# Kernel tuning notes

Hardware: AMD Instinct MI355X
Metric: run time of the kernel (lower is better)

The kernel has to match this reference:

```python
import jax, jax.numpy as jnp
import numpy as np

D_MODEL = 512
NHEAD = 8
D_K = D_MODEL // NHEAD


def setup_inputs() -> dict:
    key = jax.random.key(0)
    ks = jax.random.split(key, 11)
    B, N = 2, 16384
    s = 1.0 / np.sqrt(D_MODEL)
    inp = {
        "query": jax.random.normal(ks[0], (B, N, D_MODEL), jnp.float32),
        "key": jax.random.normal(ks[1], (B, N, D_MODEL), jnp.float32),
        "value": jax.random.normal(ks[2], (B, N, D_MODEL), jnp.float32),
        "Wq": jax.random.normal(ks[3], (D_MODEL, D_MODEL), jnp.float32) * s,
        "bq": jnp.zeros((D_MODEL,), jnp.float32),
        "Wk": jax.random.normal(ks[4], (D_MODEL, D_MODEL), jnp.float32) * s,
        "bk": jnp.zeros((D_MODEL,), jnp.float32),
        "Wv": jax.random.normal(ks[5], (D_MODEL, D_MODEL), jnp.float32) * s,
        "bv": jnp.zeros((D_MODEL,), jnp.float32),
        "Wo": jax.random.normal(ks[6], (D_MODEL, D_MODEL), jnp.float32) * s,
        "bo": jnp.zeros((D_MODEL,), jnp.float32),
    }
    return inp


def _split_heads(x):
    # [b, n, d_model] -> [b, h, n, d_k]
    b, n, _ = x.shape
    return x.reshape(b, n, NHEAD, D_K).transpose(0, 2, 1, 3)


def reference(query, key, value, Wq, bq, Wk, bk, Wv, bv, Wo, bo):
    b, n, _ = query.shape
    q = _split_heads(query @ Wq + bq)  # [b,h,n,dk]
    k = _split_heads(key @ Wk + bk)
    v = _split_heads(value @ Wv + bv)

    # linear attention (Shen et al. 2018): softmax over feature dim of q,
    # softmax over sequence dim of k, then KV outer-product context.
    q = jax.nn.softmax(q, axis=-1) / jnp.sqrt(jnp.asarray(D_K, q.dtype))
    k = jax.nn.softmax(k, axis=-2)
    context = jnp.einsum('bhnd,bhne->bhde', k, v)   # [b,h,dk,dk]
    out = jnp.einsum('bhnd,bhde->bhne', q, context)  # [b,h,n,dk]

    out = out.transpose(0, 2, 1, 3).reshape(b, n, D_MODEL)
    return out @ Wo + bo
```

## Files before the change

kernel.cpp:

```cpp
#include <hip/hip_runtime.h>
#include <hip/hip_bf16.h>


using u16 = unsigned short;
typedef __attribute__((ext_vector_type(8))) short bf16x8;
typedef __attribute__((ext_vector_type(4))) float f32x4;

#define D_MODEL 512
#define SEQ 16384


#define PART_OFF 0u
#define SUMS_OFF 16777216u
#define CTX_OFF  17039360u
#define WTKS_OFF 17301504u
#define WTVS_OFF 17825792u
#define WTQS_OFF 18350080u
#define MTS_OFF  18874368u
#define WS_NEEDED 19922944u

__device__ __forceinline__ float bf2f(u16 u) {
  union { unsigned int i; float f; } x; x.i = ((unsigned int)u) << 16; return x.f;
}
__device__ __forceinline__ u16 f2bf(float f) {
  union { float ff; unsigned int i; } x; x.ff = f;
  unsigned int r = x.i + 0x7fffu + ((x.i >> 16) & 1u);
  return (u16)(r >> 16);
}
__device__ __forceinline__ unsigned int pk2(float lo, float hi) {
  union { __hip_bfloat162 h; unsigned int u; } x;
  x.h = __float22bfloat162_rn(float2{lo, hi});
  return x.u;
}
__device__ __forceinline__ bf16x8 ldsrd(const u16* base, int row, int rowbytes,
                                        int kbyte, int mask) {
  return *(const bf16x8*)((const char*)base + row * rowbytes + (kbyte ^ ((row & mask) << 4)));
}
__device__ __forceinline__ void bar_lgkm() {
  asm volatile("s_waitcnt lgkmcnt(0)" ::: "memory");
  __builtin_amdgcn_sched_barrier(0);
  __builtin_amdgcn_s_barrier();
  __builtin_amdgcn_sched_barrier(0);
}

__launch_bounds__(256)
__global__ void wcvt_kernel(const float* __restrict__ Wk, const float* __restrict__ Wv,
                            const float* __restrict__ Wq, u16* __restrict__ WTks,
                            u16* __restrict__ WTvs, u16* __restrict__ WTqs) {
  const float* in = blockIdx.z == 0 ? Wk : (blockIdx.z == 1 ? Wv : Wq);
  u16* out = blockIdx.z == 0 ? WTks : (blockIdx.z == 1 ? WTvs : WTqs);
  __shared__ float S[64][65];
  const int t = threadIdx.x;
  const int k0 = blockIdx.y << 6, c0 = blockIdx.x << 6;
#pragma unroll
  for (int ii = 0; ii < 4; ++ii) {
    const int idx = t + ii * 256;
    const int r = idx >> 4, c4 = (idx & 15) << 2;
    const float4 v = *(const float4*)(in + (k0 + r) * D_MODEL + c0 + c4);
    S[r][c4] = v.x; S[r][c4 + 1] = v.y; S[r][c4 + 2] = v.z; S[r][c4 + 3] = v.w;
  }
  __syncthreads();
#pragma unroll
  for (int it = 0; it < 2; ++it) {
    const int fi = it * 256 + t;
    const int cb_loc = fi >> 7;
    const int ksm_loc = (fi >> 6) & 1;
    const int lane = fi & 63;
    const int col_loc = cb_loc * 16 + (lane & 15);
    const int kl0 = ksm_loc * 32 + (lane >> 4) * 8;
    union { bf16x8 v; u16 e[8]; } o;
#pragma unroll
    for (int jj = 0; jj < 8; ++jj) o.e[jj] = f2bf(S[kl0 + jj][col_loc]);
    const int cb16 = blockIdx.x * 4 + cb_loc;
    const int ksm = blockIdx.y * 2 + ksm_loc;
    *(bf16x8*)(out + cb16 * 8192 + ksm * 512 + lane * 8) = o.v;
  }
}

__launch_bounds__(512, 4)
__global__ void phase1_kernel(const float* __restrict__ key, const float* __restrict__ value,
                              const u16* __restrict__ WTks, const u16* __restrict__ WTvs,
                              const float* __restrict__ bkp, const float* __restrict__ bvp,
                              float* __restrict__ part, float* __restrict__ sums) {
  __shared__ __align__(16) u16 smem[40960];
  u16* KA = smem;
  u16* VA = smem + 16384;
  u16* ET = smem + 32768;
  u16* VT = smem + 36864;
  const int t = threadIdx.x;
  const int lane = t & 63, w = t >> 6;
  const int g = lane >> 4, lc = lane & 15;
  const int f = blockIdx.x;
  const int jj = f >> 3, xc = f & 7;
  const int hp = jj & 3;
  const int y = xc * 16 + (jj >> 2);
  const int hloc = w >> 2, cq = w & 3;
  const int h = hp * 2 + hloc;
  const int dl = cq * 16 + lc;
  const int b = y >> 6, grp = y & 63;
  const int bh = b * 8 + h;
  u16* ETh = ET + hloc * 2048;
  u16* VTh = VT + hloc * 2048;
  const u16* wtkb = WTks + (h * 4 + cq) * 8192;
  const u16* wtvb = WTvs + (h * 4 + cq) * 8192;
  const float bbk = bkp[h * 64 + dl];
  const float bbv = bvp[h * 64 + dl];
  const int srow = t >> 4, sc8 = t & 15;
  const int swoff = srow * 1024 + ((sc8 << 3) ^ ((srow & 7) << 4));

  f32x4 pacc[4];
#pragma unroll
  for (int em = 0; em < 4; ++em) pacc[em] = (f32x4){0.f, 0.f, 0.f, 0.f};
  float sp = 0.f;
  bf16x8 bB[16];

#pragma unroll 1
  for (int ci = 0; ci < 8; ++ci) {
    const int n0 = (y * 8 + ci) * 32;
    {
      const float* kp = key + (size_t)(n0 + srow) * D_MODEL + sc8 * 4;
      const float* vp = value + (size_t)(n0 + srow) * D_MODEL + sc8 * 4;
      float4 lk[8], lv[8];
#pragma unroll
      for (int q = 0; q < 8; ++q) lk[q] = *(const float4*)(kp + q * 64);
#pragma unroll
      for (int q = 0; q < 8; ++q) lv[q] = *(const float4*)(vp + q * 64);
#pragma unroll
      for (int q = 0; q < 8; ++q) {
        *(uint2*)((char*)KA + swoff + q * 128) =
            make_uint2(pk2(lk[q].x, lk[q].y), pk2(lk[q].z, lk[q].w));
        *(uint2*)((char*)VA + swoff + q * 128) =
            make_uint2(pk2(lv[q].x, lv[q].y), pk2(lv[q].z, lv[q].w));
      }
    }
    bar_lgkm();

#pragma unroll
    for (int ks = 0; ks < 16; ++ks) bB[ks] = *(const bf16x8*)(wtkb + ks * 512 + lane * 8);
    f32x4 a0 = (f32x4){0.f, 0.f, 0.f, 0.f}, a1 = a0;
#pragma unroll
    for (int ks = 0; ks < 16; ++ks) {
      const int kb = ks * 64 + g * 16;
      bf16x8 ak0 = ldsrd(KA, lc, 1024, kb, 7);
      bf16x8 ak1 = ldsrd(KA, 16 + lc, 1024, kb, 7);
      a0 = __builtin_amdgcn_mfma_f32_16x16x32_bf16(ak0, bB[ks], a0, 0, 0, 0);
      a1 = __builtin_amdgcn_mfma_f32_16x16x32_bf16(ak1, bB[ks], a1, 0, 0, 0);
    }
    {
#pragma unroll
      for (int r = 0; r < 4; ++r) { a0[r] = __expf(a0[r] + bbk); sp += a0[r]; }
#pragma unroll
      for (int r = 0; r < 4; ++r) { a1[r] = __expf(a1[r] + bbk); sp += a1[r]; }
      *(uint2*)((char*)ETh + dl * 64 + ((g * 8) ^ ((dl & 3) << 4))) =
          make_uint2(pk2(a0[0], a0[1]), pk2(a0[2], a0[3]));
      *(uint2*)((char*)ETh + dl * 64 + ((32 + g * 8) ^ ((dl & 3) << 4))) =
          make_uint2(pk2(a1[0], a1[1]), pk2(a1[2], a1[3]));
    }
#pragma unroll
    for (int ks = 0; ks < 16; ++ks) bB[ks] = *(const bf16x8*)(wtvb + ks * 512 + lane * 8);
    a0 = (f32x4){0.f, 0.f, 0.f, 0.f}; a1 = a0;
#pragma unroll
    for (int ks = 0; ks < 16; ++ks) {
      const int kb = ks * 64 + g * 16;
      bf16x8 av0 = ldsrd(VA, lc, 1024, kb, 7);
      bf16x8 av1 = ldsrd(VA, 16 + lc, 1024, kb, 7);
      a0 = __builtin_amdgcn_mfma_f32_16x16x32_bf16(av0, bB[ks], a0, 0, 0, 0);
      a1 = __builtin_amdgcn_mfma_f32_16x16x32_bf16(av1, bB[ks], a1, 0, 0, 0);
    }
    *(uint2*)((char*)VTh + dl * 64 + ((g * 8) ^ ((dl & 3) << 4))) =
        make_uint2(pk2(a0[0] + bbv, a0[1] + bbv), pk2(a0[2] + bbv, a0[3] + bbv));
    *(uint2*)((char*)VTh + dl * 64 + ((32 + g * 8) ^ ((dl & 3) << 4))) =
        make_uint2(pk2(a1[0] + bbv, a1[1] + bbv), pk2(a1[2] + bbv, a1[3] + bbv));
    bar_lgkm();

    {
      bf16x8 paf = ldsrd(ETh, dl, 64, g * 16, 3);
#pragma unroll
      for (int em = 0; em < 4; ++em) {
        bf16x8 pbf = ldsrd(VTh, em * 16 + lc, 64, g * 16, 3);
        pacc[em] = __builtin_amdgcn_mfma_f32_16x16x32_bf16(paf, pbf, pacc[em], 0, 0, 0);
      }
    }
    bar_lgkm();
  }

  float* pp = part + (size_t)(bh * 64 + grp) * 4096;
#pragma unroll
  for (int em = 0; em < 4; ++em)
    *(f32x4*)(pp + (em * 16 + lc) * 64 + cq * 16 + g * 4) = pacc[em];
  sp += __shfl_xor(sp, 16); sp += __shfl_xor(sp, 32);
  if (g == 0) sums[(size_t)(bh * 64 + grp) * 64 + dl] = sp;
}

__launch_bounds__(256)
__global__ void reduce_kernel(const float* __restrict__ part, const float* __restrict__ sums,
                              float* __restrict__ ctx) {
  __shared__ float den[64];
  const int bh = blockIdx.x;
  const int t = threadIdx.x;
  if (t < 64) {
    float s = 0.f;
    for (int gp = 0; gp < 64; ++gp) s += sums[(size_t)(bh * 64 + gp) * 64 + t];
    den[t] = s;
  }
  float4 A0 = {0,0,0,0}, A1 = {0,0,0,0}, A2 = {0,0,0,0}, A3 = {0,0,0,0};
  const float* pb = part + (size_t)bh * 64 * 4096;
  for (int gp = 0; gp < 64; ++gp) {
    const float4* q = (const float4*)(pb + gp * 4096 + t * 16);
    const float4 q0 = q[0], q1 = q[1], q2 = q[2], q3 = q[3];
    A0.x += q0.x; A0.y += q0.y; A0.z += q0.z; A0.w += q0.w;
    A1.x += q1.x; A1.y += q1.y; A1.z += q1.z; A1.w += q1.w;
    A2.x += q2.x; A2.y += q2.y; A2.z += q2.z; A2.w += q2.w;
    A3.x += q3.x; A3.y += q3.y; A3.z += q3.z; A3.w += q3.w;
  }
  __syncthreads();
  const int e = t >> 2, d0 = (t & 3) * 16;
  float* cb = ctx + (size_t)bh * 4096 + e;
  const float r0[4] = {A0.x, A0.y, A0.z, A0.w};
  const float r1[4] = {A1.x, A1.y, A1.z, A1.w};
  const float r2[4] = {A2.x, A2.y, A2.z, A2.w};
  const float r3[4] = {A3.x, A3.y, A3.z, A3.w};
#pragma unroll
  for (int i = 0; i < 4; ++i) cb[(d0 + i) * 64] = r0[i] / den[d0 + i];
#pragma unroll
  for (int i = 0; i < 4; ++i) cb[(d0 + 4 + i) * 64] = r1[i] / den[d0 + 4 + i];
#pragma unroll
  for (int i = 0; i < 4; ++i) cb[(d0 + 8 + i) * 64] = r2[i] / den[d0 + 8 + i];
#pragma unroll
  for (int i = 0; i < 4; ++i) cb[(d0 + 12 + i) * 64] = r3[i] / den[d0 + 12 + i];
}

__launch_bounds__(256)
__global__ void mbigT_kernel(const float* __restrict__ ctx, const float* __restrict__ Wo,
                             u16* __restrict__ MTs) {
  __shared__ float Clds[64][65];
  __shared__ float Wlds2[64][64];
  const int t = threadIdx.x;
  const int tx = t & 15, ty = t >> 4;
  const int cc = blockIdx.x;
  const int bh = blockIdx.y;
  const int b = bh >> 3, h = bh & 7;
  const float* ch = ctx + bh * 4096;
  for (int i4 = t; i4 < 1024; i4 += 256) {
    const int r = i4 >> 4, c = (i4 & 15) << 2;
    const float4 v = *(const float4*)(ch + (r << 6) + c);
    Clds[r][c] = v.x; Clds[r][c + 1] = v.y; Clds[r][c + 2] = v.z; Clds[r][c + 3] = v.w;
    const float4 wv = *(const float4*)(Wo + (h * 64 + r) * D_MODEL + cc * 64 + c);
    Wlds2[r][c] = wv.x; Wlds2[r][c + 1] = wv.y; Wlds2[r][c + 2] = wv.z; Wlds2[r][c + 3] = wv.w;
  }
  __syncthreads();
  float acc[4][4] = {};
#pragma unroll 8
  for (int k = 0; k < 64; ++k) {
    float a[4], wv[4];
#pragma unroll
    for (int i = 0; i < 4; ++i) a[i] = Clds[(ty << 2) + i][k];
#pragma unroll
    for (int j = 0; j < 4; ++j) wv[j] = Wlds2[k][(tx << 2) + j];
#pragma unroll
    for (int i = 0; i < 4; ++i)
#pragma unroll
      for (int j = 0; j < 4; ++j) acc[i][j] = fmaf(a[i], wv[j], acc[i][j]);
  }
#pragma unroll
  for (int i = 0; i < 4; ++i)
#pragma unroll
    for (int j = 0; j < 4; ++j) {
      const int c = cc * 64 + (tx << 2) + j;
      const int k = h * 64 + (ty << 2) + i;
      const int cb16 = c >> 4, lcc = c & 15;
      const int ksm = k >> 5, gg = (k >> 3) & 3, jb = k & 7;
      MTs[(size_t)b * 262144 + cb16 * 8192 + ksm * 512 + (gg * 16 + lcc) * 8 + jb]
          = f2bf(acc[i][j]);
    }
}

__launch_bounds__(512, 2)
__global__ void phase3_kernel(const float* __restrict__ query, const u16* __restrict__ WTqs,
                              const float* __restrict__ bqp, const u16* __restrict__ MTs,
                              const float* __restrict__ bop, float* __restrict__ out) {
  __shared__ __align__(16) u16 smem[20480];
  u16* SL = smem;
  u16* P  = smem + 4096;
  const int t = threadIdx.x;
  const int lane = t & 63, w = t >> 6;
  const int g = lane >> 4, lc = lane & 15;
  const int chunk = blockIdx.x;
  const int n0 = chunk * 32;
  const int b = chunk >> 9;
  const int c0 = w * 64;
  const int srow = t >> 4;
  const int scol = (t & 15) << 2;
  const int sbyte = srow * 128 + (((t & 15) << 3) ^ ((srow & 7) << 4));
  const float* qbase = query + (size_t)(n0 + srow) * D_MODEL + scol;

  float4 lq[2];
  f32x4 acc[4][2];
#pragma unroll
  for (int m = 0; m < 4; ++m)
#pragma unroll
    for (int n = 0; n < 2; ++n) acc[m][n] = (f32x4){0.f, 0.f, 0.f, 0.f};

  lq[0] = *(const float4*)(qbase);
  lq[1] = *(const float4*)(qbase + 64);
  *(uint2*)((char*)SL + sbyte) = make_uint2(pk2(lq[0].x, lq[0].y), pk2(lq[0].z, lq[0].w));
  bar_lgkm();

#pragma unroll
  for (int ks = 0; ks < 8; ++ks) {
    if (ks + 2 < 8) lq[ks & 1] = *(const float4*)(qbase + (ks + 2) * 64);
    if (ks + 1 < 8) {
      const int p = (ks + 1) & 1;
      *(uint2*)((char*)SL + p * 4096 + sbyte) =
          make_uint2(pk2(lq[p].x, lq[p].y), pk2(lq[p].z, lq[p].w));
    }
    const u16* S = SL + (ks & 1) * 2048;
#pragma unroll
    for (int kk = 0; kk < 2; ++kk) {
      const int ksm = ks * 2 + kk;
      bf16x8 af[4], bfr[2];
#pragma unroll
      for (int mf = 0; mf < 4; ++mf)
        af[mf] = *(const bf16x8*)(WTqs + (w * 4 + mf) * 8192 + ksm * 512 + lane * 8);
#pragma unroll
      for (int nf = 0; nf < 2; ++nf) bfr[nf] = ldsrd(S, nf * 16 + lc, 128, kk * 64 + g * 16, 7);
#pragma unroll
      for (int mf = 0; mf < 4; ++mf)
#pragma unroll
        for (int nf = 0; nf < 2; ++nf)
          acc[mf][nf] = __builtin_amdgcn_mfma_f32_16x16x32_bf16(af[mf], bfr[nf], acc[mf][nf], 0, 0, 0);
    }
    bar_lgkm();
  }
  {
    float bqv[4][4];
#pragma unroll
    for (int m = 0; m < 4; ++m)
#pragma unroll
      for (int r = 0; r < 4; ++r) bqv[m][r] = bqp[c0 + m * 16 + g * 4 + r];
#pragma unroll
    for (int nf = 0; nf < 2; ++nf) {
      float mx = -3.0e38f;
#pragma unroll
      for (int m = 0; m < 4; ++m)
#pragma unroll
        for (int r = 0; r < 4; ++r) {
          const float v = acc[m][nf][r] + bqv[m][r];
          acc[m][nf][r] = v; mx = fmaxf(mx, v);
        }
      mx = fmaxf(mx, __shfl_xor(mx, 16)); mx = fmaxf(mx, __shfl_xor(mx, 32));
      float s = 0.f;
#pragma unroll
      for (int m = 0; m < 4; ++m)
#pragma unroll
        for (int r = 0; r < 4; ++r) {
          const float e = __expf(acc[m][nf][r] - mx);
          acc[m][nf][r] = e; s += e;
        }
      s += __shfl_xor(s, 16); s += __shfl_xor(s, 32);
      const float fsc = 0.125f / s;
      const int n = nf * 16 + lc;
#pragma unroll
      for (int m = 0; m < 4; ++m) {
        const uint2 pw = make_uint2(pk2(acc[m][nf][0] * fsc, acc[m][nf][1] * fsc),
                                    pk2(acc[m][nf][2] * fsc, acc[m][nf][3] * fsc));
        *(uint2*)((char*)P + n * 1024 + ((w * 128 + m * 32 + g * 8) ^ ((n & 7) << 4))) = pw;
      }
    }
  }
  bar_lgkm();
  f32x4 oc[4][2];
#pragma unroll
  for (int m = 0; m < 4; ++m)
#pragma unroll
    for (int n = 0; n < 2; ++n) oc[m][n] = (f32x4){0.f, 0.f, 0.f, 0.f};
  const u16* MT = MTs + (size_t)b * 262144;
#pragma unroll 2
  for (int ks = 0; ks < 16; ++ks) {
    bf16x8 af[4], bfr[2];
#pragma unroll
    for (int mf = 0; mf < 4; ++mf)
      af[mf] = *(const bf16x8*)(MT + (w * 4 + mf) * 8192 + ks * 512 + lane * 8);
#pragma unroll
    for (int nf = 0; nf < 2; ++nf) bfr[nf] = ldsrd(P, nf * 16 + lc, 1024, ks * 64 + g * 16, 7);
#pragma unroll
    for (int mf = 0; mf < 4; ++mf)
#pragma unroll
      for (int nf = 0; nf < 2; ++nf)
        oc[mf][nf] = __builtin_amdgcn_mfma_f32_16x16x32_bf16(af[mf], bfr[nf], oc[mf][nf], 0, 0, 0);
  }
  {
    float bov[4][4];
#pragma unroll
    for (int m = 0; m < 4; ++m)
#pragma unroll
      for (int r = 0; r < 4; ++r) bov[m][r] = bop[c0 + m * 16 + g * 4 + r];
#pragma unroll
    for (int mf = 0; mf < 4; ++mf)
#pragma unroll
      for (int nf = 0; nf < 2; ++nf) {
        float4 o;
        o.x = oc[mf][nf][0] + bov[mf][0]; o.y = oc[mf][nf][1] + bov[mf][1];
        o.z = oc[mf][nf][2] + bov[mf][2]; o.w = oc[mf][nf][3] + bov[mf][3];
        *(float4*)(out + (size_t)(n0 + nf * 16 + lc) * D_MODEL + c0 + mf * 16 + g * 4) = o;
      }
  }
}

__global__ void sentinel_kernel(float* out) { out[0] = 1.0e9f; }

extern "C" void kernel_launch(void* const* d_in, const int* in_sizes, int n_in,
                              void* d_out, int out_size, void* d_ws, size_t ws_size,
                              hipStream_t stream) {
  const float* query = (const float*)d_in[0];
  const float* key   = (const float*)d_in[1];
  const float* value = (const float*)d_in[2];
  const float* Wq = (const float*)d_in[3];
  const float* bq = (const float*)d_in[4];
  const float* Wk = (const float*)d_in[5];
  const float* bk = (const float*)d_in[6];
  const float* Wv = (const float*)d_in[7];
  const float* bv = (const float*)d_in[8];
  const float* Wo = (const float*)d_in[9];
  const float* bo = (const float*)d_in[10];
  float* out = (float*)d_out;
  char* ws = (char*)d_ws;

  if (ws_size < (size_t)WS_NEEDED) {
    sentinel_kernel<<<1, 1, 0, stream>>>(out);
    return;
  }

  float* part = (float*)(ws + PART_OFF);
  float* sums = (float*)(ws + SUMS_OFF);
  float* ctx  = (float*)(ws + CTX_OFF);
  u16* WTks   = (u16*)(ws + WTKS_OFF);
  u16* WTvs   = (u16*)(ws + WTVS_OFF);
  u16* WTqs   = (u16*)(ws + WTQS_OFF);
  u16* MTs    = (u16*)(ws + MTS_OFF);

  const dim3 blk256(256);
  wcvt_kernel<<<dim3(8, 8, 3), blk256, 0, stream>>>(Wk, Wv, Wq, WTks, WTvs, WTqs);
  phase1_kernel<<<512, 512, 0, stream>>>(key, value, WTks, WTvs, bk, bv, part, sums);
  reduce_kernel<<<16, blk256, 0, stream>>>(part, sums, ctx);
  mbigT_kernel<<<dim3(8, 16), blk256, 0, stream>>>(ctx, Wo, MTs);
  phase3_kernel<<<1024, 512, 0, stream>>>(query, WTqs, bq, MTs, bo, out);
}
```

Measured before the change: 233.4 us.

## Split phase1 K-dim staging into 128-wide chunks and double the grid

Phase1 now stages key/value in 32x128 bf16 chunks through a much smaller LDS buffer (32KB instead of 80KB), looping over four K-chunks per 32-row tile, and raises the occupancy hint. Each block now covers half as many rows and the grid doubles to 1024 blocks, so the partial context buffer and the reduce loop grow to 128 groups. The aim is more resident blocks and more parallelism to hide global load latency. The cost is more barriers per tile, more weight reloads, and twice the partial-sum traffic in the reduce kernel.

```diff
diff --git a/kernel.cpp b/kernel.cpp
--- a/kernel.cpp
+++ b/kernel.cpp
@@ -11,13 +11,13 @@
 
 
 #define PART_OFF 0u
-#define SUMS_OFF 16777216u
-#define CTX_OFF  17039360u
-#define WTKS_OFF 17301504u
-#define WTVS_OFF 17825792u
-#define WTQS_OFF 18350080u
-#define MTS_OFF  18874368u
-#define WS_NEEDED 19922944u
+#define SUMS_OFF 33554432u
+#define CTX_OFF  34078720u
+#define WTKS_OFF 34340864u
+#define WTVS_OFF 34865152u
+#define WTQS_OFF 35389440u
+#define MTS_OFF  35913728u
+#define WS_NEEDED 36962304u
 
 __device__ __forceinline__ float bf2f(u16 u) {
   union { unsigned int i; float f; } x; x.i = ((unsigned int)u) << 16; return x.f;
@@ -77,27 +77,27 @@
   }
 }
 
-__launch_bounds__(512, 4)
+__launch_bounds__(512, 6)
 __global__ void phase1_kernel(const float* __restrict__ key, const float* __restrict__ value,
                               const u16* __restrict__ WTks, const u16* __restrict__ WTvs,
                               const float* __restrict__ bkp, const float* __restrict__ bvp,
                               float* __restrict__ part, float* __restrict__ sums) {
-  __shared__ __align__(16) u16 smem[40960];
+  __shared__ __align__(16) u16 smem[16384];
   u16* KA = smem;
-  u16* VA = smem + 16384;
-  u16* ET = smem + 32768;
-  u16* VT = smem + 36864;
+  u16* VA = smem + 4096;
+  u16* ET = smem + 8192;
+  u16* VT = smem + 12288;
   const int t = threadIdx.x;
   const int lane = t & 63, w = t >> 6;
   const int g = lane >> 4, lc = lane & 15;
   const int f = blockIdx.x;
-  const int jj = f >> 3, xc = f & 7;
-  const int hp = jj & 3;
-  const int y = xc * 16 + (jj >> 2);
+  const int xc = f & 7, kk2 = f >> 3;
+  const int rowgroup = xc * 32 + (kk2 >> 2);
+  const int hp = kk2 & 3;
   const int hloc = w >> 2, cq = w & 3;
   const int h = hp * 2 + hloc;
   const int dl = cq * 16 + lc;
-  const int b = y >> 6, grp = y & 63;
+  const int b = rowgroup >> 7, grpl = rowgroup & 127;
   const int bh = b * 8 + h;
   u16* ETh = ET + hloc * 2048;
   u16* VTh = VT + hloc * 2048;
@@ -105,72 +105,80 @@
   const u16* wtvb = WTvs + (h * 4 + cq) * 8192;
   const float bbk = bkp[h * 64 + dl];
   const float bbv = bvp[h * 64 + dl];
-  const int srow = t >> 4, sc8 = t & 15;
-  const int swoff = srow * 1024 + ((sc8 << 3) ^ ((srow & 7) << 4));
+  const int sr = t >> 4;
+  const int so8 = t & 15;
+  const int swoff = sr * 256 + ((so8 * 16) ^ ((sr & 7) << 4));
 
   f32x4 pacc[4];
 #pragma unroll
   for (int em = 0; em < 4; ++em) pacc[em] = (f32x4){0.f, 0.f, 0.f, 0.f};
   float sp = 0.f;
-  bf16x8 bB[16];
 
 #pragma unroll 1
-  for (int ci = 0; ci < 8; ++ci) {
-    const int n0 = (y * 8 + ci) * 32;
+  for (int ci = 0; ci < 4; ++ci) {
+    const int n0 = (rowgroup * 4 + ci) * 32;
+    f32x4 aK0 = (f32x4){0.f,0.f,0.f,0.f}, aK1 = aK0, aV0 = aK0, aV1 = aK0;
+
+#pragma unroll
+    for (int kq = 0; kq < 4; ++kq) {
+      if (ci > 0 || kq > 0) bar_lgkm();
+      {
+        const float* kp = key + (size_t)(n0 + sr) * D_MODEL + kq * 128 + so8 * 8;
+        const float4 k0 = *(const float4*)kp, k1 = *(const float4*)(kp + 4);
+        uint4 wk; wk.x = pk2(k0.x, k0.y); wk.y = pk2(k0.z, k0.w);
+        wk.z = pk2(k1.x, k1.y); wk.w = pk2(k1.z, k1.w);
+        *(uint4*)((char*)KA + swoff) = wk;
+        const float* vp = value + (size_t)(n0 + sr) * D_MODEL + kq * 128 + so8 * 8;
+        const float4 v0 = *(const float4*)vp, v1 = *(const float4*)(vp + 4);
+        uint4 wv; wv.x = pk2(v0.x, v0.y); wv.y = pk2(v0.z, v0.w);
+        wv.z = pk2(v1.x, v1.y); wv.w = pk2(v1.z, v1.w);
+        *(uint4*)((char*)VA + swoff) = wv;
+      }
+      bar_lgkm();
+      {
+        bf16x8 bB[4];
+#pragma unroll
+        for (int ksl = 0; ksl < 4; ++ksl)
+          bB[ksl] = *(const bf16x8*)(wtkb + (kq * 4 + ksl) * 512 + lane * 8);
+#pragma unroll
+        for (int ksl = 0; ksl < 4; ++ksl) {
+          const int kb = ksl * 64 + g * 16;
+          bf16x8 a0 = ldsrd(KA, lc, 256, kb, 7);
+          bf16x8 a1 = ldsrd(KA, 16 + lc, 256, kb, 7);
+          aK0 = __builtin_amdgcn_mfma_f32_16x16x32_bf16(a0, bB[ksl], aK0, 0, 0, 0);
+          aK1 = __builtin_amdgcn_mfma_f32_16x16x32_bf16(a1, bB[ksl], aK1, 0, 0, 0);
+        }
+      }
+      {
+        bf16x8 bB[4];
+#pragma unroll
+        for (int ksl = 0; ksl < 4; ++ksl)
+          bB[ksl] = *(const bf16x8*)(wtvb + (kq * 4 + ksl) * 512 + lane * 8);
+#pragma unroll
+        for (int ksl = 0; ksl < 4; ++ksl) {
+          const int kb = ksl * 64 + g * 16;
+          bf16x8 a0 = ldsrd(VA, lc, 256, kb, 7);
+          bf16x8 a1 = ldsrd(VA, 16 + lc, 256, kb, 7);
+          aV0 = __builtin_amdgcn_mfma_f32_16x16x32_bf16(a0, bB[ksl], aV0, 0, 0, 0);
+          aV1 = __builtin_amdgcn_mfma_f32_16x16x32_bf16(a1, bB[ksl], aV1, 0, 0, 0);
+        }
+      }
+    }
+
     {
-      const float* kp = key + (size_t)(n0 + srow) * D_MODEL + sc8 * 4;
-      const float* vp = value + (size_t)(n0 + srow) * D_MODEL + sc8 * 4;
-      float4 lk[8], lv[8];
-#pragma unroll
-      for (int q = 0; q < 8; ++q) lk[q] = *(const float4*)(kp + q * 64);
-#pragma unroll
-      for (int q = 0; q < 8; ++q) lv[q] = *(const float4*)(vp + q * 64);
-#pragma unroll
-      for (int q = 0; q < 8; ++q) {
-        *(uint2*)((char*)KA + swoff + q * 128) =
-            make_uint2(pk2(lk[q].x, lk[q].y), pk2(lk[q].z, lk[q].w));
-        *(uint2*)((char*)VA + swoff + q * 128) =
-            make_uint2(pk2(lv[q].x, lv[q].y), pk2(lv[q].z, lv[q].w));
-      }
-    }
-    bar_lgkm();
-
-#pragma unroll
-    for (int ks = 0; ks < 16; ++ks) bB[ks] = *(const bf16x8*)(wtkb + ks * 512 + lane * 8);
-    f32x4 a0 = (f32x4){0.f, 0.f, 0.f, 0.f}, a1 = a0;
-#pragma unroll
-    for (int ks = 0; ks < 16; ++ks) {
-      const int kb = ks * 64 + g * 16;
-      bf16x8 ak0 = ldsrd(KA, lc, 1024, kb, 7);
-      bf16x8 ak1 = ldsrd(KA, 16 + lc, 1024, kb, 7);
-      a0 = __builtin_amdgcn_mfma_f32_16x16x32_bf16(ak0, bB[ks], a0, 0, 0, 0);
-      a1 = __builtin_amdgcn_mfma_f32_16x16x32_bf16(ak1, bB[ks], a1, 0, 0, 0);
-    }
-    {
-#pragma unroll
-      for (int r = 0; r < 4; ++r) { a0[r] = __expf(a0[r] + bbk); sp += a0[r]; }
-#pragma unroll
-      for (int r = 0; r < 4; ++r) { a1[r] = __expf(a1[r] + bbk); sp += a1[r]; }
+#pragma unroll
+      for (int r = 0; r < 4; ++r) { aK0[r] = __expf(aK0[r] + bbk); sp += aK0[r]; }
+#pragma unroll
+      for (int r = 0; r < 4; ++r) { aK1[r] = __expf(aK1[r] + bbk); sp += aK1[r]; }
       *(uint2*)((char*)ETh + dl * 64 + ((g * 8) ^ ((dl & 3) << 4))) =
-          make_uint2(pk2(a0[0], a0[1]), pk2(a0[2], a0[3]));
+          make_uint2(pk2(aK0[0], aK0[1]), pk2(aK0[2], aK0[3]));
       *(uint2*)((char*)ETh + dl * 64 + ((32 + g * 8) ^ ((dl & 3) << 4))) =
-          make_uint2(pk2(a1[0], a1[1]), pk2(a1[2], a1[3]));
-    }
-#pragma unroll
-    for (int ks = 0; ks < 16; ++ks) bB[ks] = *(const bf16x8*)(wtvb + ks * 512 + lane * 8);
-    a0 = (f32x4){0.f, 0.f, 0.f, 0.f}; a1 = a0;
-#pragma unroll
-    for (int ks = 0; ks < 16; ++ks) {
-      const int kb = ks * 64 + g * 16;
-      bf16x8 av0 = ldsrd(VA, lc, 1024, kb, 7);
-      bf16x8 av1 = ldsrd(VA, 16 + lc, 1024, kb, 7);
-      a0 = __builtin_amdgcn_mfma_f32_16x16x32_bf16(av0, bB[ks], a0, 0, 0, 0);
-      a1 = __builtin_amdgcn_mfma_f32_16x16x32_bf16(av1, bB[ks], a1, 0, 0, 0);
+          make_uint2(pk2(aK1[0], aK1[1]), pk2(aK1[2], aK1[3]));
     }
     *(uint2*)((char*)VTh + dl * 64 + ((g * 8) ^ ((dl & 3) << 4))) =
-        make_uint2(pk2(a0[0] + bbv, a0[1] + bbv), pk2(a0[2] + bbv, a0[3] + bbv));
+        make_uint2(pk2(aV0[0] + bbv, aV0[1] + bbv), pk2(aV0[2] + bbv, aV0[3] + bbv));
     *(uint2*)((char*)VTh + dl * 64 + ((32 + g * 8) ^ ((dl & 3) << 4))) =
-        make_uint2(pk2(a1[0] + bbv, a1[1] + bbv), pk2(a1[2] + bbv, a1[3] + bbv));
+        make_uint2(pk2(aV1[0] + bbv, aV1[1] + bbv), pk2(aV1[2] + bbv, aV1[3] + bbv));
     bar_lgkm();
 
     {
@@ -184,12 +192,12 @@
     bar_lgkm();
   }
 
-  float* pp = part + (size_t)(bh * 64 + grp) * 4096;
+  float* pp = part + (size_t)(bh * 128 + grpl) * 4096;
 #pragma unroll
   for (int em = 0; em < 4; ++em)
     *(f32x4*)(pp + (em * 16 + lc) * 64 + cq * 16 + g * 4) = pacc[em];
   sp += __shfl_xor(sp, 16); sp += __shfl_xor(sp, 32);
-  if (g == 0) sums[(size_t)(bh * 64 + grp) * 64 + dl] = sp;
+  if (g == 0) sums[(size_t)(bh * 128 + grpl) * 64 + dl] = sp;
 }
 
 __launch_bounds__(256)
@@ -200,12 +208,12 @@
   const int t = threadIdx.x;
   if (t < 64) {
     float s = 0.f;
-    for (int gp = 0; gp < 64; ++gp) s += sums[(size_t)(bh * 64 + gp) * 64 + t];
+    for (int gp = 0; gp < 128; ++gp) s += sums[(size_t)(bh * 128 + gp) * 64 + t];
     den[t] = s;
   }
   float4 A0 = {0,0,0,0}, A1 = {0,0,0,0}, A2 = {0,0,0,0}, A3 = {0,0,0,0};
-  const float* pb = part + (size_t)bh * 64 * 4096;
-  for (int gp = 0; gp < 64; ++gp) {
+  const float* pb = part + (size_t)bh * 128 * 4096;
+  for (int gp = 0; gp < 128; ++gp) {
     const float4* q = (const float4*)(pb + gp * 4096 + t * 16);
     const float4 q0 = q[0], q1 = q[1], q2 = q[2], q3 = q[3];
     A0.x += q0.x; A0.y += q0.y; A0.z += q0.z; A0.w += q0.w;
@@ -441,7 +449,7 @@
 
   const dim3 blk256(256);
   wcvt_kernel<<<dim3(8, 8, 3), blk256, 0, stream>>>(Wk, Wv, Wq, WTks, WTvs, WTqs);
-  phase1_kernel<<<512, 512, 0, stream>>>(key, value, WTks, WTvs, bk, bv, part, sums);
+  phase1_kernel<<<1024, 512, 0, stream>>>(key, value, WTks, WTvs, bk, bv, part, sums);
   reduce_kernel<<<16, blk256, 0, stream>>>(part, sums, ctx);
   mbigT_kernel<<<dim3(8, 16), blk256, 0, stream>>>(ctx, Wo, MTs);
   phase3_kernel<<<1024, 512, 0, stream>>>(query, WTqs, bq, MTs, bo, out);
```

Result: slower. 317.1 us (+35.9%).
